# Kernel tuning notes

Measured on AMD Instinct MI355X. Metric: run time of the kernel, lower is better.

Reference implementation:

```python
import math
import jax, jax.numpy as jnp
import numpy as np

D_MODEL = 1024
N_HEAD = 16
HEAD_DIM = D_MODEL // N_HEAD
THETA = 10000.0


def precompute_rope(seq_len, head_dim):
    half = head_dim // 2
    inv_freq = 1.0 / (THETA ** (jnp.arange(half, dtype=jnp.float32) / half))
    pos = jnp.arange(seq_len, dtype=jnp.float32)
    freqs = jnp.outer(pos, inv_freq)  # [S, half]
    return jnp.cos(freqs), jnp.sin(freqs)


def apply_rope(x, cos, sin):
    # x: [B, H, S, Dh]; cos/sin: [S, Dh//2] -> broadcast over B, H
    x_even = x[..., 0::2]
    x_odd = x[..., 1::2]
    cos = cos[None, None]
    sin = sin[None, None]
    out_even = x_even * cos - x_odd * sin
    out_odd = x_even * sin + x_odd * cos
    # interleave back: stack on last axis then flatten pairs
    return jnp.stack((out_even, out_odd), axis=-1).reshape(x.shape)


def setup_inputs() -> dict:
    key = jax.random.key(0)
    kx, kq, kp = jax.random.split(key, 3)
    x = jax.random.normal(kx, (4, 2048, D_MODEL), dtype=jnp.float32)
    s = 1.0 / math.sqrt(D_MODEL)
    # torch Linear weight is [out, in]; we store transposed [in, out] for x @ W
    W_qkv = jax.random.normal(kq, (D_MODEL, 3 * D_MODEL), dtype=jnp.float32) * s
    W_proj = jax.random.normal(kp, (D_MODEL, D_MODEL), dtype=jnp.float32) * s
    return {"x": x, "W_qkv": W_qkv, "W_proj": W_proj}


def reference(x, W_qkv, W_proj):
    bsz, seqlen, d_model = x.shape
    qkv = x @ W_qkv  # [B, S, 3D]
    q, k, v = jnp.split(qkv, 3, axis=-1)
    def to_heads(t):
        return t.reshape(bsz, seqlen, N_HEAD, HEAD_DIM).transpose(0, 2, 1, 3)
    q, k, v = to_heads(q), to_heads(k), to_heads(v)  # [B, H, S, Dh]
    cos, sin = precompute_rope(seqlen, HEAD_DIM)
    q = apply_rope(q, cos, sin)
    k = apply_rope(k, cos, sin)
    att = jnp.einsum('bhqd,bhkd->bhqk', q, k) * (1.0 / math.sqrt(HEAD_DIM))
    causal = jnp.tril(jnp.ones((seqlen, seqlen), dtype=bool))
    att = jnp.where(causal[None, None], att, -jnp.inf)
    att = jax.nn.softmax(att, axis=-1)
    y = jnp.einsum('bhqk,bhkd->bhqd', att, v)
    y = y.transpose(0, 2, 1, 3).reshape(bsz, seqlen, d_model)
    return y @ W_proj
```

## Files before the change

kernel.cpp:

```cpp
#include <hip/hip_runtime.h>


#define BATCH 4
#define SEQ   2048
#define DM    1024
#define NH    16
#define HD    64
#define QKV_W 3072

typedef short bf16x8 __attribute__((ext_vector_type(8)));
typedef float f32x4  __attribute__((ext_vector_type(4)));
typedef unsigned short bf16_t;

__device__ __forceinline__ unsigned short f2bf(float f) {
  unsigned u = __float_as_uint(f);
  u += 0x7fffu + ((u >> 16) & 1u);
  return (unsigned short)(u >> 16);
}
__device__ __forceinline__ float bf2f(unsigned short s) {
  return __uint_as_float((unsigned)s << 16);
}
__device__ __forceinline__ void gld16(const void* g, void* l) {
  __builtin_amdgcn_global_load_lds(
      (const __attribute__((address_space(1))) unsigned int*)g,
      (__attribute__((address_space(3))) unsigned int*)l, 16, 0, 0);
}

__global__ __launch_bounds__(256) void k_transpose(const float* __restrict__ W,
                                                   bf16_t* __restrict__ Wt,
                                                   int K, int N) {
  __shared__ float tile[32][33];
  const int tx = threadIdx.x, ty = threadIdx.y;
  const int n0 = blockIdx.x * 32, k0 = blockIdx.y * 32;
#pragma unroll
  for (int j = 0; j < 4; ++j)
    tile[ty + j * 8][tx] = W[(size_t)(k0 + ty + j * 8) * N + n0 + tx];
  __syncthreads();
#pragma unroll
  for (int j = 0; j < 4; ++j)
    Wt[(size_t)(n0 + ty + j * 8) * K + k0 + tx] = f2bf(tile[tx][ty + j * 8]);
}

__global__ __launch_bounds__(256) void k_cvt(const float* __restrict__ x,
                                             bf16_t* __restrict__ xb) {
  const int i = (blockIdx.x * 256 + threadIdx.x) * 4;
  float4 v = *(const float4*)(x + i);
  unsigned lo = (unsigned)f2bf(v.x) | ((unsigned)f2bf(v.y) << 16);
  unsigned hi = (unsigned)f2bf(v.z) | ((unsigned)f2bf(v.w) << 16);
  *(uint2*)(xb + i) = make_uint2(lo, hi);
}

__global__ __launch_bounds__(256) void k_rope(bf16_t* __restrict__ qkv) {
  const int t = blockIdx.x * 256 + threadIdx.x;
  const int i = t & 31;
  const int h = (t >> 5) & 15;
  const int s = (t >> 9) & 2047;
  const int b = t >> 20;
  const float inv = __expf((float)i * -0.28782313662425575f);
  float sn, cs;
  sincosf((float)s * inv, &sn, &cs);
  size_t base = ((size_t)(b * SEQ + s)) * QKV_W + h * HD + 2 * i;
#pragma unroll
  for (int part = 0; part < 2; ++part) {
    unsigned u = *(unsigned*)(qkv + base + part * DM);
    float e = bf2f((unsigned short)(u & 0xffffu));
    float o = bf2f((unsigned short)(u >> 16));
    unsigned short e2 = f2bf(e * cs - o * sn);
    unsigned short o2 = f2bf(e * sn + o * cs);
    *(unsigned*)(qkv + base + part * DM) = (unsigned)e2 | ((unsigned)o2 << 16);
  }
}

template<int MODE>
__global__ __launch_bounds__(256) void k_gemm(const bf16_t* __restrict__ A,
                                              const bf16_t* __restrict__ Bt,
                                              void* __restrict__ Cout,
                                              bf16_t* __restrict__ vt,
                                              int M, int N, int K) {
  __shared__ __align__(16) short As[128 * 64];
  __shared__ __align__(16) short Bs[128 * 64];
  const int tid = threadIdx.x;
  const int wave = tid >> 6, lane = tid & 63;
  const int quad = lane >> 4, l16 = lane & 15;
  const int wm = (wave >> 1) * 64, wn = (wave & 1) * 64;
  const int bm = blockIdx.y * 128, bn = blockIdx.x * 128;

  f32x4 acc[4][4];
#pragma unroll
  for (int i = 0; i < 4; ++i)
#pragma unroll
    for (int j = 0; j < 4; ++j) acc[i][j] = f32x4{0.f, 0.f, 0.f, 0.f};

  const int srow = tid >> 3;
  const int sg   = (tid & 7) ^ (srow & 7);
  const bf16_t* Ap = A  + (size_t)(bm + srow) * K + sg * 8;
  const bf16_t* Bp = Bt + (size_t)(bn + srow) * K + sg * 8;
  short* Ad = As + tid * 8;
  short* Bd = Bs + tid * 8;

  for (int k0 = 0; k0 < K; k0 += 64) {
    __syncthreads();
#pragma unroll
    for (int pp = 0; pp < 4; ++pp) {
      gld16(Ap + (size_t)(pp * 32) * K + k0, Ad + pp * 2048);
      gld16(Bp + (size_t)(pp * 32) * K + k0, Bd + pp * 2048);
    }
    __syncthreads();
#pragma unroll
    for (int ks = 0; ks < 2; ++ks) {
      bf16x8 af[4], bfr[4];
#pragma unroll
      for (int i = 0; i < 4; ++i)
        af[i] = *(const bf16x8*)&As[(wm + i * 16 + l16) * 64 +
                                    (((ks * 4 + quad) ^ (l16 & 7)) << 3)];
#pragma unroll
      for (int j = 0; j < 4; ++j)
        bfr[j] = *(const bf16x8*)&Bs[(wn + j * 16 + l16) * 64 +
                                     (((ks * 4 + quad) ^ (l16 & 7)) << 3)];
#pragma unroll
      for (int i = 0; i < 4; ++i)
#pragma unroll
        for (int j = 0; j < 4; ++j)
          acc[i][j] = __builtin_amdgcn_mfma_f32_16x16x32_bf16(af[i], bfr[j], acc[i][j], 0, 0, 0);
    }
  }
#pragma unroll
  for (int i = 0; i < 4; ++i)
#pragma unroll
    for (int j = 0; j < 4; ++j) {
      const int col = bn + wn + j * 16 + l16;
      const int row0 = bm + wm + i * 16 + quad * 4;
      if (MODE == 1 && col >= 2048) {
        const int d = col - 2048;
        const int hh = d >> 6, dd = d & 63;
        const int bb = row0 >> 11, ss = row0 & 2047;
        ushort4 pk;
        pk.x = f2bf(acc[i][j][0]); pk.y = f2bf(acc[i][j][1]);
        pk.z = f2bf(acc[i][j][2]); pk.w = f2bf(acc[i][j][3]);
        *(ushort4*)(vt + ((size_t)((bb * NH + hh) * HD + dd)) * SEQ + ss) = pk;
      } else {
#pragma unroll
        for (int r = 0; r < 4; ++r) {
          if (MODE == 1)
            ((bf16_t*)Cout)[(size_t)(row0 + r) * N + col] = f2bf(acc[i][j][r]);
          else
            ((float*)Cout)[(size_t)(row0 + r) * N + col] = acc[i][j][r];
        }
      }
    }
}

#define QSCALE 0.18033688011112042f
__global__ __launch_bounds__(256, 2) void k_attn(const bf16_t* __restrict__ qkv,
                                                 const bf16_t* __restrict__ vt,
                                                 bf16_t* __restrict__ y) {
  __shared__ __align__(16) short KV[2][4][64 * 32];
  __shared__ __align__(16) short Pb[4][32 * 64];
  const int tid = threadIdx.x;
  const int wave = tid >> 6, lane = tid & 63;
  const int quad = lane >> 4, l16 = lane & 15;
  const int l = blockIdx.x;
  const int p = (l >> 3) & 7;
  const int g = ((l >> 6) << 3) | (l & 7);
  const int h = g & 15, b = g >> 4;
  const size_t bbase = (size_t)b * SEQ * QKV_W;
  short* Pw = &Pb[wave][0];
  const int srow = tid >> 2;
  const int sc8  = (tid & 3) * 8;
  const bf16_t* kbase = qkv + bbase + (size_t)srow * QKV_W + DM + h * HD + sc8;
  const bf16_t* vbase = vt + ((size_t)(b * NH + h) * HD + srow) * SEQ + sc8;

#define ISSUE(kv0, buf)                                              \
  do {                                                               \
    gld16(kbase + (size_t)(kv0) * QKV_W,      &KV[buf][0][tid * 8]); \
    gld16(kbase + (size_t)(kv0) * QKV_W + 32, &KV[buf][1][tid * 8]); \
    gld16(vbase + (kv0),                      &KV[buf][2][tid * 8]); \
    gld16(vbase + (kv0) + 32,                 &KV[buf][3][tid * 8]); \
  } while (0)

  int bufp = 0;
  ISSUE(0, 0);
  for (int half = 0; half < 2; ++half) {
    const int qt = half ? (15 - p) : p;
    const int qb = qt * 128 + wave * 32;
    bf16x8 aq[2][2];
#pragma unroll
    for (int mi = 0; mi < 2; ++mi)
#pragma unroll
      for (int kk = 0; kk < 2; ++kk) {
        const bf16_t* qp = qkv + bbase + (size_t)(qb + mi * 16 + l16) * QKV_W +
                           h * HD + kk * 32 + quad * 8;
        bf16x8 raw = *(const bf16x8*)qp;
        bf16x8 sc;
#pragma unroll
        for (int e = 0; e < 8; ++e)
          sc[e] = (short)f2bf(bf2f((unsigned short)raw[e]) * QSCALE);
        aq[mi][kk] = sc;
      }
    f32x4 o[2][4];
    float lsum[2][4];
#pragma unroll
    for (int mi = 0; mi < 2; ++mi)
#pragma unroll
      for (int jn = 0; jn < 4; ++jn) o[mi][jn] = f32x4{0.f, 0.f, 0.f, 0.f};
#pragma unroll
    for (int mi = 0; mi < 2; ++mi)
#pragma unroll
      for (int r = 0; r < 4; ++r) lsum[mi][r] = 0.f;

    const int jmax = 2 * qt + 1;
    for (int j = 0; j <= jmax; ++j) {
      const int kv0 = j * 64;
      __syncthreads();
      if (j < jmax)          ISSUE(kv0 + 64, bufp ^ 1);
      else if (half == 0)    ISSUE(0, bufp ^ 1);
      if (kv0 <= qb + 31) {
        const bool needmask = (kv0 + 63 > qb);
        const short* Kc0 = &KV[bufp][0][0];
        const short* Kc1 = &KV[bufp][1][0];
        const short* Vc0 = &KV[bufp][2][0];
        const short* Vc1 = &KV[bufp][3][0];

        f32x4 sacc[2][4];
#pragma unroll
        for (int jn = 0; jn < 4; ++jn) {
          bf16x8 bk0 = *(const bf16x8*)&Kc0[(jn * 16 + l16) * 32 + quad * 8];
          bf16x8 bk1 = *(const bf16x8*)&Kc1[(jn * 16 + l16) * 32 + quad * 8];
#pragma unroll
          for (int mi = 0; mi < 2; ++mi) {
            f32x4 s4 = f32x4{0.f, 0.f, 0.f, 0.f};
            s4 = __builtin_amdgcn_mfma_f32_16x16x32_bf16(aq[mi][0], bk0, s4, 0, 0, 0);
            s4 = __builtin_amdgcn_mfma_f32_16x16x32_bf16(aq[mi][1], bk1, s4, 0, 0, 0);
            sacc[mi][jn] = s4;
          }
        }
#pragma unroll
        for (int mi = 0; mi < 2; ++mi)
#pragma unroll
          for (int r = 0; r < 4; ++r) {
            const int prow = mi * 16 + quad * 4 + r;
            const int qr = qb + prow;
#pragma unroll
            for (int jn = 0; jn < 4; ++jn) {
              float e = __builtin_amdgcn_exp2f(sacc[mi][jn][r]);
              if (needmask) e = (kv0 + jn * 16 + l16 <= qr) ? e : 0.f;
              lsum[mi][r] += e;
              const int pcol = jn * 16 + l16;
              Pw[prow * 64 + ((((pcol >> 3) ^ (prow & 7))) << 3) + (pcol & 7)] =
                  (short)(__float_as_uint(e) >> 16);
            }
          }
#pragma unroll
        for (int ks = 0; ks < 2; ++ks) {
          const int gsw = ((ks * 4 + quad) ^ (l16 & 7)) << 3;
          bf16x8 ap0 = *(const bf16x8*)&Pw[l16 * 64 + gsw];
          bf16x8 ap1 = *(const bf16x8*)&Pw[(16 + l16) * 64 + gsw];
          const short* Vc = ks ? Vc1 : Vc0;
#pragma unroll
          for (int jn = 0; jn < 4; ++jn) {
            bf16x8 bv = *(const bf16x8*)&Vc[(jn * 16 + l16) * 32 + quad * 8];
            o[0][jn] = __builtin_amdgcn_mfma_f32_16x16x32_bf16(ap0, bv, o[0][jn], 0, 0, 0);
            o[1][jn] = __builtin_amdgcn_mfma_f32_16x16x32_bf16(ap1, bv, o[1][jn], 0, 0, 0);
          }
        }
      }
      bufp ^= 1;
    }
#pragma unroll
    for (int mi = 0; mi < 2; ++mi)
#pragma unroll
      for (int r = 0; r < 4; ++r) {
        float s = lsum[mi][r];
        s += __shfl_xor(s, 1, 64);
        s += __shfl_xor(s, 2, 64);
        s += __shfl_xor(s, 4, 64);
        s += __shfl_xor(s, 8, 64);
        const float invl = 1.0f / s;
        const int qr = qb + mi * 16 + quad * 4 + r;
        bf16_t* yp = y + ((size_t)b * SEQ + qr) * DM + h * HD;
#pragma unroll
        for (int jn = 0; jn < 4; ++jn)
          yp[jn * 16 + l16] = f2bf(o[mi][jn][r] * invl);
      }
  }
#undef ISSUE
}

extern "C" void kernel_launch(void* const* d_in, const int* in_sizes, int n_in,
                              void* d_out, int out_size, void* d_ws, size_t ws_size,
                              hipStream_t stream) {
  const float* x     = (const float*)d_in[0];
  const float* Wqkv  = (const float*)d_in[1];
  const float* Wproj = (const float*)d_in[2];
  float* out = (float*)d_out;
  char* ws = (char*)d_ws;
  bf16_t* qkv = (bf16_t*)(ws);
  bf16_t* Wt1 = (bf16_t*)(ws + 50331648);
  bf16_t* Wt2 = (bf16_t*)(ws + 56623104);
  bf16_t* xb  = (bf16_t*)(ws + 58720256);
  bf16_t* y   = xb;
  bf16_t* vt  = (bf16_t*)d_out;

  k_transpose<<<dim3(QKV_W / 32, DM / 32), dim3(32, 8), 0, stream>>>(Wqkv, Wt1, DM, QKV_W);
  k_transpose<<<dim3(DM / 32, DM / 32), dim3(32, 8), 0, stream>>>(Wproj, Wt2, DM, DM);
  k_cvt<<<(BATCH * SEQ * DM) / (4 * 256), 256, 0, stream>>>(x, xb);
  k_gemm<1><<<dim3(QKV_W / 128, (BATCH * SEQ) / 128), 256, 0, stream>>>(
      xb, Wt1, qkv, vt, BATCH * SEQ, QKV_W, DM);
  k_rope<<<(BATCH * SEQ * NH * 32) / 256, 256, 0, stream>>>(qkv);
  k_attn<<<512, 256, 0, stream>>>(qkv, vt, y);
  k_gemm<0><<<dim3(DM / 128, (BATCH * SEQ) / 128), 256, 0, stream>>>(
      y, Wt2, out, nullptr, BATCH * SEQ, DM, DM);
}
```

Before: 264.6 us.

## Load K/V fragments directly from global memory, dropping shared-memory staging

The attention kernel no longer stages K and V tiles through double-buffered shared memory with async global-to-LDS loads and block-wide barriers. Each wave now reads its K and V MFMA operand fragments straight from global memory into registers and runs its own causal loop bound. Launch bounds go to 3 blocks per SM. This removes the __syncthreads and LDS traffic and lets waves skip tiles independently, but the four waves in a block now each reload the same K/V data from global/L2 and get no prefetch overlap.

```diff
diff --git a/kernel.cpp b/kernel.cpp
--- a/kernel.cpp
+++ b/kernel.cpp
@@ -151,10 +151,9 @@
 }
 
 #define QSCALE 0.18033688011112042f
-__global__ __launch_bounds__(256, 2) void k_attn(const bf16_t* __restrict__ qkv,
+__global__ __launch_bounds__(256, 3) void k_attn(const bf16_t* __restrict__ qkv,
                                                  const bf16_t* __restrict__ vt,
                                                  bf16_t* __restrict__ y) {
-  __shared__ __align__(16) short KV[2][4][64 * 32];
   __shared__ __align__(16) short Pb[4][32 * 64];
   const int tid = threadIdx.x;
   const int wave = tid >> 6, lane = tid & 63;
@@ -165,21 +164,9 @@
   const int h = g & 15, b = g >> 4;
   const size_t bbase = (size_t)b * SEQ * QKV_W;
   short* Pw = &Pb[wave][0];
-  const int srow = tid >> 2;
-  const int sc8  = (tid & 3) * 8;
-  const bf16_t* kbase = qkv + bbase + (size_t)srow * QKV_W + DM + h * HD + sc8;
-  const bf16_t* vbase = vt + ((size_t)(b * NH + h) * HD + srow) * SEQ + sc8;
-
-#define ISSUE(kv0, buf)                                              \
-  do {                                                               \
-    gld16(kbase + (size_t)(kv0) * QKV_W,      &KV[buf][0][tid * 8]); \
-    gld16(kbase + (size_t)(kv0) * QKV_W + 32, &KV[buf][1][tid * 8]); \
-    gld16(vbase + (kv0),                      &KV[buf][2][tid * 8]); \
-    gld16(vbase + (kv0) + 32,                 &KV[buf][3][tid * 8]); \
-  } while (0)
-
-  int bufp = 0;
-  ISSUE(0, 0);
+  const bf16_t* kfb = qkv + bbase + (size_t)l16 * QKV_W + DM + h * HD + quad * 8;
+  const bf16_t* vfb = vt + ((size_t)(b * NH + h) * HD + l16) * SEQ + quad * 8;
+
   for (int half = 0; half < 2; ++half) {
     const int qt = half ? (15 - p) : p;
     const int qb = qt * 128 + wave * 32;
@@ -208,63 +195,59 @@
 #pragma unroll
       for (int r = 0; r < 4; ++r) lsum[mi][r] = 0.f;
 
-    const int jmax = 2 * qt + 1;
-    for (int j = 0; j <= jmax; ++j) {
+    const int jlim = (qb + 31) >> 6;
+    for (int j = 0; j <= jlim; ++j) {
       const int kv0 = j * 64;
-      __syncthreads();
-      if (j < jmax)          ISSUE(kv0 + 64, bufp ^ 1);
-      else if (half == 0)    ISSUE(0, bufp ^ 1);
-      if (kv0 <= qb + 31) {
-        const bool needmask = (kv0 + 63 > qb);
-        const short* Kc0 = &KV[bufp][0][0];
-        const short* Kc1 = &KV[bufp][1][0];
-        const short* Vc0 = &KV[bufp][2][0];
-        const short* Vc1 = &KV[bufp][3][0];
-
-        f32x4 sacc[2][4];
+      const bool needmask = (kv0 + 63 > qb);
+      bf16x8 kf[2][4];
+#pragma unroll
+      for (int ks = 0; ks < 2; ++ks)
+#pragma unroll
+        for (int jn = 0; jn < 4; ++jn)
+          kf[ks][jn] = *(const bf16x8*)(kfb + (size_t)(kv0 + jn * 16) * QKV_W + ks * 32);
+      f32x4 sacc[2][4];
+#pragma unroll
+      for (int jn = 0; jn < 4; ++jn)
+#pragma unroll
+        for (int mi = 0; mi < 2; ++mi) {
+          f32x4 s4 = f32x4{0.f, 0.f, 0.f, 0.f};
+          s4 = __builtin_amdgcn_mfma_f32_16x16x32_bf16(aq[mi][0], kf[0][jn], s4, 0, 0, 0);
+          s4 = __builtin_amdgcn_mfma_f32_16x16x32_bf16(aq[mi][1], kf[1][jn], s4, 0, 0, 0);
+          sacc[mi][jn] = s4;
+        }
+      bf16x8 vf[2][4];
+#pragma unroll
+      for (int ks = 0; ks < 2; ++ks)
+#pragma unroll
+        for (int jn = 0; jn < 4; ++jn)
+          vf[ks][jn] = *(const bf16x8*)(vfb + (size_t)(jn * 16) * SEQ + kv0 + ks * 32);
+#pragma unroll
+      for (int mi = 0; mi < 2; ++mi)
+#pragma unroll
+        for (int r = 0; r < 4; ++r) {
+          const int prow = mi * 16 + quad * 4 + r;
+          const int qr = qb + prow;
+#pragma unroll
+          for (int jn = 0; jn < 4; ++jn) {
+            float e = __builtin_amdgcn_exp2f(sacc[mi][jn][r]);
+            if (needmask) e = (kv0 + jn * 16 + l16 <= qr) ? e : 0.f;
+            lsum[mi][r] += e;
+            const int pcol = jn * 16 + l16;
+            Pw[prow * 64 + ((((pcol >> 3) ^ (prow & 7))) << 3) + (pcol & 7)] =
+                (short)(__float_as_uint(e) >> 16);
+          }
+        }
+#pragma unroll
+      for (int ks = 0; ks < 2; ++ks) {
+        const int gsw = ((ks * 4 + quad) ^ (l16 & 7)) << 3;
+        bf16x8 ap0 = *(const bf16x8*)&Pw[l16 * 64 + gsw];
+        bf16x8 ap1 = *(const bf16x8*)&Pw[(16 + l16) * 64 + gsw];
 #pragma unroll
         for (int jn = 0; jn < 4; ++jn) {
-          bf16x8 bk0 = *(const bf16x8*)&Kc0[(jn * 16 + l16) * 32 + quad * 8];
-          bf16x8 bk1 = *(const bf16x8*)&Kc1[(jn * 16 + l16) * 32 + quad * 8];
-#pragma unroll
-          for (int mi = 0; mi < 2; ++mi) {
-            f32x4 s4 = f32x4{0.f, 0.f, 0.f, 0.f};
-            s4 = __builtin_amdgcn_mfma_f32_16x16x32_bf16(aq[mi][0], bk0, s4, 0, 0, 0);
-            s4 = __builtin_amdgcn_mfma_f32_16x16x32_bf16(aq[mi][1], bk1, s4, 0, 0, 0);
-            sacc[mi][jn] = s4;
-          }
-        }
-#pragma unroll
-        for (int mi = 0; mi < 2; ++mi)
-#pragma unroll
-          for (int r = 0; r < 4; ++r) {
-            const int prow = mi * 16 + quad * 4 + r;
-            const int qr = qb + prow;
-#pragma unroll
-            for (int jn = 0; jn < 4; ++jn) {
-              float e = __builtin_amdgcn_exp2f(sacc[mi][jn][r]);
-              if (needmask) e = (kv0 + jn * 16 + l16 <= qr) ? e : 0.f;
-              lsum[mi][r] += e;
-              const int pcol = jn * 16 + l16;
-              Pw[prow * 64 + ((((pcol >> 3) ^ (prow & 7))) << 3) + (pcol & 7)] =
-                  (short)(__float_as_uint(e) >> 16);
-            }
-          }
-#pragma unroll
-        for (int ks = 0; ks < 2; ++ks) {
-          const int gsw = ((ks * 4 + quad) ^ (l16 & 7)) << 3;
-          bf16x8 ap0 = *(const bf16x8*)&Pw[l16 * 64 + gsw];
-          bf16x8 ap1 = *(const bf16x8*)&Pw[(16 + l16) * 64 + gsw];
-          const short* Vc = ks ? Vc1 : Vc0;
-#pragma unroll
-          for (int jn = 0; jn < 4; ++jn) {
-            bf16x8 bv = *(const bf16x8*)&Vc[(jn * 16 + l16) * 32 + quad * 8];
-            o[0][jn] = __builtin_amdgcn_mfma_f32_16x16x32_bf16(ap0, bv, o[0][jn], 0, 0, 0);
-            o[1][jn] = __builtin_amdgcn_mfma_f32_16x16x32_bf16(ap1, bv, o[1][jn], 0, 0, 0);
-          }
-        }
-      }
-      bufp ^= 1;
+          o[0][jn] = __builtin_amdgcn_mfma_f32_16x16x32_bf16(ap0, vf[ks][jn], o[0][jn], 0, 0, 0);
+          o[1][jn] = __builtin_amdgcn_mfma_f32_16x16x32_bf16(ap1, vf[ks][jn], o[1][jn], 0, 0, 0);
+        }
+      }
     }
 #pragma unroll
     for (int mi = 0; mi < 2; ++mi)
@@ -283,7 +266,6 @@
           yp[jn * 16 + l16] = f2bf(o[mi][jn][r] * invl);
       }
   }
-#undef ISSUE
 }
 
 extern "C" void kernel_launch(void* const* d_in, const int* in_sizes, int n_in,
```

Result: slower. 331.1 us (+25.1%).
